# Optimization experiments

Hardware: AMD Instinct MI355X
Metric: run time of the kernel (lower is better)

Reference implementation:

```python
import jax, jax.numpy as jnp
import numpy as np

H, D = 16, 64  # heads, d_head
ROPE_BASE = 10000.0


def _rotate_half(x):
    # '... (d r) -> ... d r' with r=2, unbind, cat(-x2, x1)
    xs = x.reshape(*x.shape[:-1], D // 2, 2)
    x1, x2 = xs[..., 0], xs[..., 1]
    return jnp.concatenate([-x2, x1], axis=-1)


def _rope_sin_cos(n):
    inv_freq = 1.0 / (ROPE_BASE ** (jnp.arange(0, D, 2, dtype=jnp.float32) / D))  # [D/2]
    f = jnp.arange(n, dtype=jnp.float32)[:, None] * inv_freq                      # [n, D/2]
    emb = jnp.concatenate([f, f], axis=-1)                                        # [n, D]
    # cache = cat(sin(emb), cos(emb)); apply slices sin=[:D], cos=[D:]
    return jnp.sin(emb), jnp.cos(emb)


def setup_inputs() -> dict:
    key = jax.random.key(0)
    ks = jax.random.split(key, 5)
    B, N, E = 2, 2048, 1024
    C = H * D
    s = 0.02
    return {
        "x": jax.random.normal(ks[0], (B, N, E), jnp.float32),
        "Wq": jax.random.normal(ks[1], (C, E), jnp.float32) * s,
        "bq": jnp.zeros((C,), jnp.float32),
        "Wk": jax.random.normal(ks[2], (C, E), jnp.float32) * s,
        "bk": jnp.zeros((C,), jnp.float32),
        "Wv": jax.random.normal(ks[3], (C, E), jnp.float32) * s,
        "bv": jnp.zeros((C,), jnp.float32),
        "Wo": jax.random.normal(ks[4], (E, C), jnp.float32) * s,
        "bo": jnp.zeros((E,), jnp.float32),
    }


def reference(x, Wq, bq, Wk, bk, Wv, bv, Wo, bo):
    B, N, E = x.shape

    def proj(W, b):  # [B,N,E] -> [B,H,N,D]
        y = x @ W.T + b
        return y.reshape(B, N, H, D).transpose(0, 2, 1, 3)

    q, k, v = proj(Wq, bq), proj(Wk, bk), proj(Wv, bv)

    sin, cos = _rope_sin_cos(N)  # each [N, D], broadcast over [B,H,N,D]
    q = q * cos + _rotate_half(q) * sin
    k = k * cos + _rotate_half(k) * sin

    scale = 1.0 / jnp.sqrt(jnp.float32(D))
    scores = jnp.einsum('bhqd,bhkd->bhqk', q, k) * scale  # [B,H,N,N]
    causal = jnp.tril(jnp.ones((N, N), dtype=bool))
    scores = jnp.where(causal, scores, jnp.float32(-jnp.inf))
    probs = jax.nn.softmax(scores, axis=-1)
    out = jnp.einsum('bhqk,bhkd->bhqd', probs, v)
    out = out.transpose(0, 2, 1, 3).reshape(B, N, H * D)
    return out @ Wo.T + bo
```

## Files before the change

kernel.cpp:

```cpp
#include <hip/hip_runtime.h>
#include <hip/hip_bf16.h>
#include <cstdint>
#include <cstddef>

using bf16x8 = __attribute__((ext_vector_type(8))) __bf16;
using f32x4  = __attribute__((ext_vector_type(4))) float;

__device__ __forceinline__ float b2f(unsigned short u) {
  union { unsigned u; float f; } x; x.u = ((unsigned)u) << 16; return x.f;
}
__device__ __forceinline__ unsigned short f2b(float f) {
  union { float f; unsigned u; } x; x.f = f;
  unsigned r = x.u + 0x7fffu + ((x.u >> 16) & 1u);
  return (unsigned short)(r >> 16);
}
__device__ __forceinline__ unsigned short f2b_trunc(float f) {
  union { float f; unsigned u; } x; x.f = f;
  return (unsigned short)(x.u >> 16);
}

__device__ __forceinline__ void gload_lds16(const void* g, void* l) {
  __builtin_amdgcn_global_load_lds(
      (const __attribute__((address_space(1))) void*)g,
      (__attribute__((address_space(3))) void*)l, 16, 0, 0);
}

__device__ __forceinline__ bf16x8 ldfrag(const unsigned short* p) {
  return *reinterpret_cast<const bf16x8*>(p);
}

__global__ __launch_bounds__(256) void cast_all_kernel(const float* __restrict__ x,
                                                       const float* __restrict__ Wq,
                                                       const float* __restrict__ Wk,
                                                       const float* __restrict__ Wv,
                                                       const float* __restrict__ Wo,
                                                       unsigned short* __restrict__ xb,
                                                       unsigned short* __restrict__ wqkv,
                                                       unsigned short* __restrict__ wob) {
  const int i = blockIdx.x * 256 + threadIdx.x;
  const int XW = 1048576;
  const int WW = 262144;
  const float* s; unsigned short* d; int j;
  if (i < XW)                { s = x;  d = xb;              j = i; }
  else if (i < XW + WW)      { s = Wq; d = wqkv;            j = i - XW; }
  else if (i < XW + 2 * WW)  { s = Wk; d = wqkv + 1048576;  j = i - XW - WW; }
  else if (i < XW + 3 * WW)  { s = Wv; d = wqkv + 2097152;  j = i - XW - 2 * WW; }
  else                       { s = Wo; d = wob;             j = i - XW - 3 * WW; }
  float4 v = reinterpret_cast<const float4*>(s)[j];
  ushort4 o;
  o.x = f2b(v.x); o.y = f2b(v.y); o.z = f2b(v.z); o.w = f2b(v.w);
  reinterpret_cast<ushort4*>(d)[j] = o;
}

__global__ __launch_bounds__(256) void sincos_kernel(float* __restrict__ st,
                                                     float* __restrict__ ct, int total) {
  int i = blockIdx.x * 256 + threadIdx.x;
  if (i >= total) return;
  int n = i >> 5, j = i & 31;
  float inv = powf(10000.0f, -(float)j * (1.0f / 32.0f));
  float ang = (float)n * inv;
  st[i] = sinf(ang);
  ct[i] = cosf(ang);
}

__global__ __launch_bounds__(512) void gemm256(const unsigned short* __restrict__ A,
                                               const unsigned short* __restrict__ B,
                                               unsigned short* __restrict__ Qo,
                                               unsigned short* __restrict__ Ko,
                                               unsigned short* __restrict__ Vt,
                                               const float* __restrict__ st,
                                               const float* __restrict__ ct,
                                               const float* __restrict__ bq,
                                               const float* __restrict__ bk,
                                               const float* __restrict__ bv,
                                               int M, int N, int K, int TN) {
  extern __shared__ __align__(16) unsigned short sm[];
  const int tid = threadIdx.x, lane = tid & 63, wave = tid >> 6;
  const int lr = lane & 15, lk = lane >> 4;
  const int wr = wave >> 2, wc = wave & 3;

  int wg = (int)blockIdx.x;
  const int cpx = (int)gridDim.x >> 3;
  wg = (wg & 7) * cpx + (wg >> 3);
  const int bn = (wg % TN) * 192, bm = (wg / TN) * 256;

  const int srow = wave * 8 + (lane >> 3);
  const int scol = (((lane & 7) * 16) ^ (((lane >> 3) & 7) << 4)) >> 1;
  const unsigned short* Ag = A + (size_t)(bm + srow) * K + scol;
  const unsigned short* Bg = B + (size_t)(bn + srow) * K + scol;

  auto issueA = [&](int kt, int nb, int i) {
    gload_lds16(Ag + (size_t)(i * 64) * K + (size_t)kt * 64,
                sm + nb * 28672 + wave * 512 + i * 4096);
  };
  auto issueB = [&](int kt, int nb, int i) {
    gload_lds16(Bg + (size_t)(i * 64) * K + (size_t)kt * 64,
                sm + nb * 28672 + 16384 + wave * 512 + i * 4096);
  };

  f32x4 acc[8][3] = {};
  const int swz = (lr & 7) << 4;
  const int NT = K / 64;

#pragma unroll
  for (int i = 0; i < 3; ++i) issueB(0, 0, i);
#pragma unroll
  for (int i = 0; i < 4; ++i) issueA(0, 0, i);
  asm volatile("s_waitcnt vmcnt(0)" ::: "memory");
  __builtin_amdgcn_s_barrier();

  for (int kt = 0; kt < NT; ++kt) {
    const int cur = kt & 1, nb = cur ^ 1;
    const bool pf = (kt + 1 < NT);

    const unsigned short* Ab = sm + cur * 28672 + wr * 8192;
    const unsigned short* Bb = sm + cur * 28672 + 16384;

    bf16x8 b[3][2];
#pragma unroll
    for (int n = 0; n < 3; ++n)
#pragma unroll
      for (int kk = 0; kk < 2; ++kk)
        b[n][kk] = ldfrag(&Bb[(wc * 48 + n * 16 + lr) * 64 + (((kk * 64 + lk * 16) ^ swz) >> 1)]);

#pragma unroll
    for (int q = 0; q < 4; ++q) {
      if (q == 2) {
        if (pf) asm volatile("s_waitcnt vmcnt(4)" ::: "memory");
        else    asm volatile("s_waitcnt vmcnt(0)" ::: "memory");
        __builtin_amdgcn_s_barrier();
      }
      if (pf) {
        if (q == 0)      { issueB(kt + 1, nb, 0); issueB(kt + 1, nb, 1); }
        else if (q == 1) { issueB(kt + 1, nb, 2); issueA(kt + 1, nb, 0); }
        else if (q == 2) { issueA(kt + 1, nb, 1); issueA(kt + 1, nb, 2); }
        else             { issueA(kt + 1, nb, 3); }
      }
      bf16x8 a[2][2];
#pragma unroll
      for (int m = 0; m < 2; ++m)
#pragma unroll
        for (int kk = 0; kk < 2; ++kk)
          a[m][kk] = ldfrag(&Ab[((q * 2 + m) * 16 + lr) * 64 + (((kk * 64 + lk * 16) ^ swz) >> 1)]);
      __builtin_amdgcn_s_barrier();
      __builtin_amdgcn_s_setprio(1);
#pragma unroll
      for (int kk = 0; kk < 2; ++kk)
#pragma unroll
        for (int m = 0; m < 2; ++m)
#pragma unroll
          for (int n = 0; n < 3; ++n)
            acc[q * 2 + m][n] =
                __builtin_amdgcn_mfma_f32_16x16x32_bf16(a[m][kk], b[n][kk], acc[q * 2 + m][n], 0, 0, 0);
      __builtin_amdgcn_s_setprio(0);
      if (q < 3) __builtin_amdgcn_s_barrier();
    }

    if (pf) {
      asm volatile("s_waitcnt vmcnt(1)" ::: "memory");
      __builtin_amdgcn_s_barrier();
    }
  }

  __syncthreads();

  const int btok = bm >> 11;
  const int ntok0 = bm & 2047;

#pragma unroll
  for (int n = 0; n < 3; ++n) {
    const int col = bn + wc * 48 + n * 16 + lr;
    if (col >= 2048) {
      const int vcol = col - 2048;
      const float bvv = bv[vcol];
      const int h = vcol >> 6, d = vcol & 63;
      unsigned short* vrow = Vt + ((size_t)((btok * 16 + h) * 64 + d)) * 2048;
#pragma unroll
      for (int mu = 0; mu < 4; ++mu) {
        uint4 w;
        w.x = (unsigned)f2b(acc[2 * mu][n][0] + bvv)     | ((unsigned)f2b(acc[2 * mu][n][1] + bvv) << 16);
        w.y = (unsigned)f2b(acc[2 * mu][n][2] + bvv)     | ((unsigned)f2b(acc[2 * mu][n][3] + bvv) << 16);
        w.z = (unsigned)f2b(acc[2 * mu + 1][n][0] + bvv) | ((unsigned)f2b(acc[2 * mu + 1][n][1] + bvv) << 16);
        w.w = (unsigned)f2b(acc[2 * mu + 1][n][2] + bvv) | ((unsigned)f2b(acc[2 * mu + 1][n][3] + bvv) << 16);
        const int ncol = ntok0 + wr * 128 + mu * 32 + 8 * lk;
        *reinterpret_cast<uint4*>(vrow + ncol) = w;
      }
    } else {
      const float bvv = (col < 1024) ? bq[col] : bk[col & 1023];
      const int lcol = wc * 48 + n * 16 + lr;
#pragma unroll
      for (int m = 0; m < 8; ++m)
#pragma unroll
        for (int r = 0; r < 4; ++r) {
          const int lrow = wr * 128 + m * 16 + lk * 4 + r;
          const int g2 = (lcol >> 3) ^ (lrow & 7);
          sm[lrow * 192 + (g2 << 3) + (lcol & 7)] = f2b(acc[m][n][r] + bvv);
        }
    }
  }
  __syncthreads();

  const int nqk = min(3, max(0, (2048 - bn) >> 6));
  for (int t = tid; t < 256 * nqk; t += 512) {
    const int hh = t >> 8, row = t & 255;
    const int ntok = ntok0 + row;
    const int col0 = bn + hh * 64;
    const bool isq = col0 < 1024;
    const int h = (col0 & 1023) >> 6;
    const float* ctp = ct + ntok * 32;
    const float* stp = st + ntok * 32;
    unsigned short xr[64];
#pragma unroll
    for (int i = 0; i < 8; ++i) {
      const int g = (hh * 8 + i) ^ (row & 7);
      *reinterpret_cast<int4*>(&xr[i * 8]) =
          *reinterpret_cast<const int4*>(&sm[row * 192 + g * 8]);
    }
    unsigned short out[64];
#pragma unroll
    for (int i = 0; i < 32; ++i) {
      const float c = ctp[i], s = stp[i];
      float o1 = b2f(xr[i]) * c - b2f(xr[2 * i + 1]) * s;
      float o2 = b2f(xr[32 + i]) * c + b2f(xr[2 * i]) * s;
      if (isq) { o1 *= 0.18033688f; o2 *= 0.18033688f; }
      out[i] = f2b(o1);
      out[32 + i] = f2b(o2);
    }
    unsigned short* dst =
        (isq ? Qo : Ko) + ((size_t)((btok * 16 + h) * 2048 + ntok)) * 64;
#pragma unroll
    for (int i = 0; i < 8; ++i)
      *reinterpret_cast<int4*>(dst + i * 8) =
          *reinterpret_cast<const int4*>(&out[i * 8]);
  }
}

template <int OUTF32>
__global__ __launch_bounds__(256) void gemm_bt(const unsigned short* __restrict__ A,
                                               const unsigned short* __restrict__ B,
                                               void* __restrict__ C,
                                               const float* __restrict__ bias,
                                               int M, int N, int K) {
  __shared__ __align__(16) unsigned short As[128 * 32];
  __shared__ __align__(16) unsigned short Bs[128 * 32];
  const int tid = threadIdx.x;
  const int lane = tid & 63, wave = tid >> 6;
  const int wr = wave >> 1, wc = wave & 1;
  const int bm = blockIdx.y * 128, bn = blockIdx.x * 128;
  const int lr = lane & 15, lk = lane >> 4;
  f32x4 acc[4][4] = {};

  for (int k0 = 0; k0 < K; k0 += 32) {
#pragma unroll
    for (int i = 0; i < 2; ++i) {
      int idx = i * 256 + tid;
      int row = idx >> 2, c8 = (idx & 3) * 8;
      gload_lds16(A + (size_t)(bm + row) * K + k0 + c8, &As[(i * 256 + wave * 64) * 8]);
      gload_lds16(B + (size_t)(bn + row) * K + k0 + c8, &Bs[(i * 256 + wave * 64) * 8]);
    }
    __syncthreads();
    bf16x8 af[4], bfr[4];
#pragma unroll
    for (int mi = 0; mi < 4; ++mi)
      af[mi] = ldfrag(&As[(wr * 64 + mi * 16 + lr) * 32 + lk * 8]);
#pragma unroll
    for (int ni = 0; ni < 4; ++ni)
      bfr[ni] = ldfrag(&Bs[(wc * 64 + ni * 16 + lr) * 32 + lk * 8]);
#pragma unroll
    for (int mi = 0; mi < 4; ++mi)
#pragma unroll
      for (int ni = 0; ni < 4; ++ni)
        acc[mi][ni] = __builtin_amdgcn_mfma_f32_16x16x32_bf16(af[mi], bfr[ni], acc[mi][ni], 0, 0, 0);
    __syncthreads();
  }

#pragma unroll
  for (int mi = 0; mi < 4; ++mi) {
#pragma unroll
    for (int ni = 0; ni < 4; ++ni) {
      int col = bn + wc * 64 + ni * 16 + lr;
      float bv = bias ? bias[col] : 0.0f;
#pragma unroll
      for (int r = 0; r < 4; ++r) {
        int row = bm + wr * 64 + mi * 16 + lk * 4 + r;
        float v = acc[mi][ni][r] + bv;
        if (OUTF32)
          reinterpret_cast<float*>(C)[(size_t)row * N + col] = v;
        else
          reinterpret_cast<unsigned short*>(C)[(size_t)row * N + col] = f2b(v);
      }
    }
  }
}

__global__ __launch_bounds__(512) void flash_kernel(const unsigned short* __restrict__ Q,
                                                    const unsigned short* __restrict__ Kb,
                                                    const unsigned short* __restrict__ Vt,
                                                    unsigned short* __restrict__ Out, int N) {
  extern __shared__ __align__(16) unsigned short smem[];
  unsigned short* KsB = smem;
  unsigned short* VsB = smem + 16384;

  const int tid = threadIdx.x;
  const int lane = tid & 63, wave = tid >> 6;
  const int lr = lane & 15, lk = lane >> 4;
  const int bh = blockIdx.x;
  const int x = blockIdx.y;
  const int qtA = x, qtB = 15 - x;
  const int ntA = x + 1;
  const unsigned short* Qh = Q + (size_t)bh * N * 64;
  const unsigned short* Kh = Kb + (size_t)bh * N * 64;
  const unsigned short* Vh = Vt + (size_t)bh * 64 * N;

  const int wrowA = qtA * 128 + wave * 16;
  const int wrowB = qtB * 128 + wave * 16;

  const int kr = tid >> 3;
  const int kcb = ((tid & 7) * 16) ^ ((kr & 7) << 4);
  const unsigned short* Kg0 = Kh + (size_t)kr * 64 + (kcb >> 1);
  const int vr = tid >> 4;
  const int vcb = ((tid & 15) * 16) ^ ((vr & 7) << 4);
  const unsigned short* Vg0 = Vh + (size_t)vr * N + (vcb >> 1);

  auto stage = [&](int buf, int tk) {
    const unsigned short* kp = Kg0 + (size_t)tk * 8192;
    const unsigned short* vp = Vg0 + (size_t)tk * 128;
    unsigned short* kl = KsB + buf * 8192 + wave * 512;
    unsigned short* vl = VsB + buf * 8192 + wave * 512;
    gload_lds16(kp, kl);
    gload_lds16(kp + 4096, kl + 4096);
    gload_lds16(vp, vl);
    gload_lds16(vp + (size_t)32 * N, vl + 4096);
  };

  stage(0, 0);

  bf16x8 qA0 = ldfrag(&Qh[(size_t)(wrowA + lr) * 64 + lk * 8]);
  bf16x8 qA1 = ldfrag(&Qh[(size_t)(wrowA + lr) * 64 + 32 + lk * 8]);
  bf16x8 qB0 = ldfrag(&Qh[(size_t)(wrowB + lr) * 64 + lk * 8]);
  bf16x8 qB1 = ldfrag(&Qh[(size_t)(wrowB + lr) * 64 + 32 + lk * 8]);

  bf16x8 ones;
  {
    union { unsigned short u; __bf16 b; } one; one.u = 0x3F80;
#pragma unroll
    for (int j = 0; j < 8; ++j) ones[j] = one.b;
  }

  const float NEG = -1e30f;
  f32x4 oacc[4] = {};
  f32x4 lacc = {};
  float m_run = NEG;

  auto compute_phase = [&](int buf, bf16x8 q0, bf16x8 q1, bool diag) {
    const unsigned short* Ksb = KsB + buf * 8192;
    const unsigned short* Vsb = VsB + buf * 8192;
    f32x4 s[8];
#pragma unroll
    for (int ni = 0; ni < 8; ++ni) s[ni] = f32x4{0.f, 0.f, 0.f, 0.f};
    __builtin_amdgcn_s_setprio(1);
#pragma unroll
    for (int ni = 0; ni < 8; ++ni) {
      const int R = ni * 16 + lr;
      const int sw = (R & 7) << 4;
      bf16x8 kf0 = ldfrag(&Ksb[R * 64 + (((lk * 16) ^ sw) >> 1)]);
      bf16x8 kf1 = ldfrag(&Ksb[R * 64 + (((64 + lk * 16) ^ sw) >> 1)]);
      s[ni] = __builtin_amdgcn_mfma_f32_16x16x32_bf16(kf0, q0, s[ni], 0, 0, 0);
      s[ni] = __builtin_amdgcn_mfma_f32_16x16x32_bf16(kf1, q1, s[ni], 0, 0, 0);
    }
    __builtin_amdgcn_s_setprio(0);

    if (diag) {
      const int ql = wave * 16 + lr;
#pragma unroll
      for (int ni = 0; ni < 8; ++ni)
#pragma unroll
        for (int r = 0; r < 4; ++r)
          if (ni * 16 + lk * 4 + r > ql) s[ni][r] = NEG;
    }

    float mx = s[0][0];
#pragma unroll
    for (int ni = 0; ni < 8; ++ni)
#pragma unroll
      for (int r = 0; r < 4; ++r)
        if (ni || r) mx = fmaxf(mx, s[ni][r]);
    mx = fmaxf(mx, __shfl_xor(mx, 16, 64));
    mx = fmaxf(mx, __shfl_xor(mx, 32, 64));

    if (!__all(mx - m_run <= 8.0f)) {
      float nm = fmaxf(m_run, mx);
      float alpha = __builtin_amdgcn_exp2f(m_run - nm);
      m_run = nm;
#pragma unroll
      for (int ni = 0; ni < 4; ++ni) oacc[ni] *= alpha;
      lacc *= alpha;
    }

    unsigned pk[8][2];
#pragma unroll
    for (int ni = 0; ni < 8; ++ni) {
      float p0 = __builtin_amdgcn_exp2f(s[ni][0] - m_run);
      float p1 = __builtin_amdgcn_exp2f(s[ni][1] - m_run);
      float p2 = __builtin_amdgcn_exp2f(s[ni][2] - m_run);
      float p3 = __builtin_amdgcn_exp2f(s[ni][3] - m_run);
      pk[ni][0] = (unsigned)f2b_trunc(p0) | ((unsigned)f2b_trunc(p1) << 16);
      pk[ni][1] = (unsigned)f2b_trunc(p2) | ((unsigned)f2b_trunc(p3) << 16);
    }

    __builtin_amdgcn_s_setprio(1);
#pragma unroll
    for (int c = 0; c < 4; ++c) {
      union { unsigned u[4]; bf16x8 v; } pb;
      pb.u[0] = pk[2 * c][0];
      pb.u[1] = pk[2 * c][1];
      pb.u[2] = pk[2 * c + 1][0];
      pb.u[3] = pk[2 * c + 1][1];
      lacc = __builtin_amdgcn_mfma_f32_16x16x32_bf16(ones, pb.v, lacc, 0, 0, 0);
      const int cb = c * 64 + lk * 16;
#pragma unroll
      for (int ni = 0; ni < 4; ++ni) {
        const int RV = ni * 16 + lr;
        bf16x8 vf = ldfrag(&Vsb[RV * 128 + ((cb ^ ((RV & 7) << 4)) >> 1)]);
        oacc[ni] = __builtin_amdgcn_mfma_f32_16x16x32_bf16(vf, pb.v, oacc[ni], 0, 0, 0);
      }
    }
    __builtin_amdgcn_s_setprio(0);
  };

  const int b = bh >> 4, h = bh & 15;
  auto epilogue = [&](int wrow0) {
    const float rl = 1.0f / lacc[0];
    const int q = wrow0 + lr;
#pragma unroll
    for (int ni = 0; ni < 4; ++ni) {
      uint2 w;
      w.x = (unsigned)f2b(oacc[ni][0] * rl) | ((unsigned)f2b(oacc[ni][1] * rl) << 16);
      w.y = (unsigned)f2b(oacc[ni][2] * rl) | ((unsigned)f2b(oacc[ni][3] * rl) << 16);
      *reinterpret_cast<uint2*>(
          &Out[((size_t)(b * N + q)) * 1024 + h * 64 + ni * 16 + lk * 4]) = w;
    }
  };

  __syncthreads();

  int buf = 0;
  for (int p = 0; p < 17; ++p) {
    if (p + 1 < 17) {
      int tk2 = (p + 1 < ntA) ? (p + 1) : (p + 1 - ntA);
      stage(buf ^ 1, tk2);
    }
    if (p == ntA) {
      epilogue(wrowA);
#pragma unroll
      for (int ni = 0; ni < 4; ++ni) oacc[ni] = f32x4{0.f, 0.f, 0.f, 0.f};
      lacc = f32x4{0.f, 0.f, 0.f, 0.f};
      m_run = NEG;
    }
    if (p < ntA) compute_phase(buf, qA0, qA1, p == ntA - 1);
    else         compute_phase(buf, qB0, qB1, p == 16);
    __syncthreads();
    buf ^= 1;
  }
  epilogue(wrowB);
}

extern "C" void kernel_launch(void* const* d_in, const int* in_sizes, int n_in,
                              void* d_out, int out_size, void* d_ws, size_t ws_size,
                              hipStream_t stream) {
  const int B = 2, N = 2048, E = 1024, C = 1024, NC = 3072;
  const int M = B * N;

  const float* x  = (const float*)d_in[0];
  const float* Wq = (const float*)d_in[1];
  const float* bq = (const float*)d_in[2];
  const float* Wk = (const float*)d_in[3];
  const float* bk = (const float*)d_in[4];
  const float* Wv = (const float*)d_in[5];
  const float* bv = (const float*)d_in[6];
  const float* Wo = (const float*)d_in[7];
  const float* bo = (const float*)d_in[8];

  char* w = (char*)d_ws;
  size_t off = 0;
  auto alloc = [&](size_t bytes) {
    void* p = w + off;
    off += (bytes + 255) & ~(size_t)255;
    return p;
  };
  unsigned short* xb    = (unsigned short*)alloc((size_t)M * E * 2);
  unsigned short* wqkv  = (unsigned short*)alloc((size_t)NC * E * 2);
  unsigned short* wob   = (unsigned short*)alloc((size_t)E * C * 2);
  unsigned short* qb    = (unsigned short*)alloc((size_t)B * 16 * N * 64 * 2);
  unsigned short* kb    = (unsigned short*)alloc((size_t)B * 16 * N * 64 * 2);
  unsigned short* vt    = (unsigned short*)alloc((size_t)B * 16 * 64 * N * 2);
  unsigned short* attnb = (unsigned short*)alloc((size_t)M * C * 2);
  float* sin_t = (float*)alloc((size_t)N * 32 * 4);
  float* cos_t = (float*)alloc((size_t)N * 32 * 4);

  cast_all_kernel<<<8192, 256, 0, stream>>>(x, Wq, Wk, Wv, Wo, xb, wqkv, wob);

  int n3 = N * 32;
  sincos_kernel<<<(n3 + 255) / 256, 256, 0, stream>>>(sin_t, cos_t, n3);

  static const int GEMM_LDS = 114688;
  hipFuncSetAttribute(reinterpret_cast<const void*>(gemm256),
                      hipFuncAttributeMaxDynamicSharedMemorySize, GEMM_LDS);
  gemm256<<<dim3((NC / 192) * (M / 256)), 512, GEMM_LDS, stream>>>(
      xb, wqkv, qb, kb, vt, sin_t, cos_t, bq, bk, bv, M, NC, E, NC / 192);

  static const int FLASH_LDS = 65536;
  hipFuncSetAttribute(reinterpret_cast<const void*>(flash_kernel),
                      hipFuncAttributeMaxDynamicSharedMemorySize, FLASH_LDS);
  flash_kernel<<<dim3(B * 16, 8), 512, FLASH_LDS, stream>>>(qb, kb, vt, attnb, N);

  gemm_bt<1><<<dim3(E / 128, M / 128), 256, 0, stream>>>(attnb, wob, d_out, bo, M, E, C);
}
```

Baseline: 112.9 us.

## Shrink QKV GEMM tile to 128x192 with 4 waves and simpler double buffering

New measurement: 121.8 us. +7.8%, slower.

```diff
diff --git a/kernel.cpp b/kernel.cpp
--- a/kernel.cpp
+++ b/kernel.cpp
@@ -63,7 +63,7 @@
   ct[i] = cosf(ang);
 }
 
-__global__ __launch_bounds__(512) void gemm256(const unsigned short* __restrict__ A,
+__global__ __launch_bounds__(256) void gemm256(const unsigned short* __restrict__ A,
                                                const unsigned short* __restrict__ B,
                                                unsigned short* __restrict__ Qo,
                                                unsigned short* __restrict__ Ko,
@@ -77,87 +77,69 @@
   extern __shared__ __align__(16) unsigned short sm[];
   const int tid = threadIdx.x, lane = tid & 63, wave = tid >> 6;
   const int lr = lane & 15, lk = lane >> 4;
-  const int wr = wave >> 2, wc = wave & 3;
+  const int wr = wave >> 1, wc = wave & 1;
 
   int wg = (int)blockIdx.x;
   const int cpx = (int)gridDim.x >> 3;
   wg = (wg & 7) * cpx + (wg >> 3);
-  const int bn = (wg % TN) * 192, bm = (wg / TN) * 256;
-
-  const int srow = wave * 8 + (lane >> 3);
-  const int scol = (((lane & 7) * 16) ^ (((lane >> 3) & 7) << 4)) >> 1;
+  const int bn = (wg % TN) * 192, bm = (wg / TN) * 128;
+
+  const int srow = tid >> 3;
+  const int scol = (((tid & 7) * 16) ^ ((srow & 7) << 4)) >> 1;
   const unsigned short* Ag = A + (size_t)(bm + srow) * K + scol;
   const unsigned short* Bg = B + (size_t)(bn + srow) * K + scol;
 
-  auto issueA = [&](int kt, int nb, int i) {
-    gload_lds16(Ag + (size_t)(i * 64) * K + (size_t)kt * 64,
-                sm + nb * 28672 + wave * 512 + i * 4096);
+  auto stage = [&](int kt, int nb) {
+    const size_t ko = (size_t)kt * 64;
+    unsigned short* base = sm + nb * 20480 + wave * 512;
+#pragma unroll
+    for (int i = 0; i < 4; ++i)
+      gload_lds16(Ag + (size_t)(i * 32) * K + ko, base + i * 2048);
+#pragma unroll
+    for (int i = 0; i < 6; ++i)
+      gload_lds16(Bg + (size_t)(i * 32) * K + ko, base + 8192 + i * 2048);
   };
-  auto issueB = [&](int kt, int nb, int i) {
-    gload_lds16(Bg + (size_t)(i * 64) * K + (size_t)kt * 64,
-                sm + nb * 28672 + 16384 + wave * 512 + i * 4096);
-  };
-
-  f32x4 acc[8][3] = {};
+
+  f32x4 acc[4][6] = {};
   const int swz = (lr & 7) << 4;
   const int NT = K / 64;
 
-#pragma unroll
-  for (int i = 0; i < 3; ++i) issueB(0, 0, i);
-#pragma unroll
-  for (int i = 0; i < 4; ++i) issueA(0, 0, i);
+  stage(0, 0);
   asm volatile("s_waitcnt vmcnt(0)" ::: "memory");
   __builtin_amdgcn_s_barrier();
 
   for (int kt = 0; kt < NT; ++kt) {
-    const int cur = kt & 1, nb = cur ^ 1;
+    const int cur = kt & 1;
     const bool pf = (kt + 1 < NT);
-
-    const unsigned short* Ab = sm + cur * 28672 + wr * 8192;
-    const unsigned short* Bb = sm + cur * 28672 + 16384;
-
-    bf16x8 b[3][2];
-#pragma unroll
-    for (int n = 0; n < 3; ++n)
+    if (pf) stage(kt + 1, cur ^ 1);
+
+    const unsigned short* Ab = sm + cur * 20480 + (size_t)wr * 64 * 64;
+    const unsigned short* Bb = sm + cur * 20480 + 8192;
+
+    bf16x8 b[6][2];
+#pragma unroll
+    for (int n = 0; n < 6; ++n)
 #pragma unroll
       for (int kk = 0; kk < 2; ++kk)
-        b[n][kk] = ldfrag(&Bb[(wc * 48 + n * 16 + lr) * 64 + (((kk * 64 + lk * 16) ^ swz) >> 1)]);
-
-#pragma unroll
-    for (int q = 0; q < 4; ++q) {
-      if (q == 2) {
-        if (pf) asm volatile("s_waitcnt vmcnt(4)" ::: "memory");
-        else    asm volatile("s_waitcnt vmcnt(0)" ::: "memory");
-        __builtin_amdgcn_s_barrier();
-      }
-      if (pf) {
-        if (q == 0)      { issueB(kt + 1, nb, 0); issueB(kt + 1, nb, 1); }
-        else if (q == 1) { issueB(kt + 1, nb, 2); issueA(kt + 1, nb, 0); }
-        else if (q == 2) { issueA(kt + 1, nb, 1); issueA(kt + 1, nb, 2); }
-        else             { issueA(kt + 1, nb, 3); }
-      }
-      bf16x8 a[2][2];
-#pragma unroll
-      for (int m = 0; m < 2; ++m)
-#pragma unroll
-        for (int kk = 0; kk < 2; ++kk)
-          a[m][kk] = ldfrag(&Ab[((q * 2 + m) * 16 + lr) * 64 + (((kk * 64 + lk * 16) ^ swz) >> 1)]);
-      __builtin_amdgcn_s_barrier();
+        b[n][kk] = ldfrag(&Bb[(wc * 96 + n * 16 + lr) * 64 + (((kk * 64 + lk * 16) ^ swz) >> 1)]);
+
+#pragma unroll
+    for (int m = 0; m < 4; ++m) {
+      bf16x8 a[2];
+#pragma unroll
+      for (int kk = 0; kk < 2; ++kk)
+        a[kk] = ldfrag(&Ab[(m * 16 + lr) * 64 + (((kk * 64 + lk * 16) ^ swz) >> 1)]);
       __builtin_amdgcn_s_setprio(1);
 #pragma unroll
       for (int kk = 0; kk < 2; ++kk)
 #pragma unroll
-        for (int m = 0; m < 2; ++m)
-#pragma unroll
-          for (int n = 0; n < 3; ++n)
-            acc[q * 2 + m][n] =
-                __builtin_amdgcn_mfma_f32_16x16x32_bf16(a[m][kk], b[n][kk], acc[q * 2 + m][n], 0, 0, 0);
+        for (int n = 0; n < 6; ++n)
+          acc[m][n] = __builtin_amdgcn_mfma_f32_16x16x32_bf16(a[kk], b[n][kk], acc[m][n], 0, 0, 0);
       __builtin_amdgcn_s_setprio(0);
-      if (q < 3) __builtin_amdgcn_s_barrier();
     }
 
     if (pf) {
-      asm volatile("s_waitcnt vmcnt(1)" ::: "memory");
+      asm volatile("s_waitcnt vmcnt(0)" ::: "memory");
       __builtin_amdgcn_s_barrier();
     }
   }
@@ -168,31 +150,31 @@
   const int ntok0 = bm & 2047;
 
 #pragma unroll
-  for (int n = 0; n < 3; ++n) {
-    const int col = bn + wc * 48 + n * 16 + lr;
+  for (int n = 0; n < 6; ++n) {
+    const int col = bn + wc * 96 + n * 16 + lr;
     if (col >= 2048) {
       const int vcol = col - 2048;
       const float bvv = bv[vcol];
       const int h = vcol >> 6, d = vcol & 63;
       unsigned short* vrow = Vt + ((size_t)((btok * 16 + h) * 64 + d)) * 2048;
 #pragma unroll
-      for (int mu = 0; mu < 4; ++mu) {
+      for (int mu = 0; mu < 2; ++mu) {
         uint4 w;
         w.x = (unsigned)f2b(acc[2 * mu][n][0] + bvv)     | ((unsigned)f2b(acc[2 * mu][n][1] + bvv) << 16);
         w.y = (unsigned)f2b(acc[2 * mu][n][2] + bvv)     | ((unsigned)f2b(acc[2 * mu][n][3] + bvv) << 16);
         w.z = (unsigned)f2b(acc[2 * mu + 1][n][0] + bvv) | ((unsigned)f2b(acc[2 * mu + 1][n][1] + bvv) << 16);
         w.w = (unsigned)f2b(acc[2 * mu + 1][n][2] + bvv) | ((unsigned)f2b(acc[2 * mu + 1][n][3] + bvv) << 16);
-        const int ncol = ntok0 + wr * 128 + mu * 32 + 8 * lk;
+        const int ncol = ntok0 + wr * 64 + mu * 32 + 8 * lk;
         *reinterpret_cast<uint4*>(vrow + ncol) = w;
       }
     } else {
       const float bvv = (col < 1024) ? bq[col] : bk[col & 1023];
-      const int lcol = wc * 48 + n * 16 + lr;
-#pragma unroll
-      for (int m = 0; m < 8; ++m)
+      const int lcol = wc * 96 + n * 16 + lr;
+#pragma unroll
+      for (int m = 0; m < 4; ++m)
 #pragma unroll
         for (int r = 0; r < 4; ++r) {
-          const int lrow = wr * 128 + m * 16 + lk * 4 + r;
+          const int lrow = wr * 64 + m * 16 + lk * 4 + r;
           const int g2 = (lcol >> 3) ^ (lrow & 7);
           sm[lrow * 192 + (g2 << 3) + (lcol & 7)] = f2b(acc[m][n][r] + bvv);
         }
@@ -201,8 +183,8 @@
   __syncthreads();
 
   const int nqk = min(3, max(0, (2048 - bn) >> 6));
-  for (int t = tid; t < 256 * nqk; t += 512) {
-    const int hh = t >> 8, row = t & 255;
+  for (int t = tid; t < 128 * nqk; t += 256) {
+    const int hh = t >> 7, row = t & 127;
     const int ntok = ntok0 + row;
     const int col0 = bn + hh * 64;
     const bool isq = col0 < 1024;
@@ -503,10 +485,10 @@
   int n3 = N * 32;
   sincos_kernel<<<(n3 + 255) / 256, 256, 0, stream>>>(sin_t, cos_t, n3);
 
-  static const int GEMM_LDS = 114688;
+  static const int GEMM_LDS = 81920;
   hipFuncSetAttribute(reinterpret_cast<const void*>(gemm256),
                       hipFuncAttributeMaxDynamicSharedMemorySize, GEMM_LDS);
-  gemm256<<<dim3((NC / 192) * (M / 256)), 512, GEMM_LDS, stream>>>(
+  gemm256<<<dim3((NC / 192) * (M / 128)), 256, GEMM_LDS, stream>>>(
       xb, wqkv, qb, kb, vt, sin_t, cos_t, bq, bk, bv, M, NC, E, NC / 192);
 
   static const int FLASH_LDS = 65536;
```
